# Optimization experiments

Measured on AMD Instinct MI355X. Metric: run time of the kernel, lower is better.

The kernel has to match this reference:

```python
import jax, jax.numpy as jnp
import numpy as np

EPS = 1e-5
PROJ_EPS = 1e-5
MAX_TANH_ARG = 15.0
NUM_LAYERS = 2

def _norm(x):
    return jnp.sqrt(jnp.sum(x * x, axis=-1, keepdims=True))

def log_map_zero(y):
    # Poincare ball log map at the origin: arctanh(||y||) * y / ||y||
    n = _norm(y)
    n_c = jnp.clip(n, EPS, 1.0 - PROJ_EPS)
    return jnp.arctanh(n_c) * y / jnp.maximum(n, EPS)

def exp_map_zero(v):
    # Poincare ball exp map at the origin: tanh(||v||) * v / ||v||
    n = _norm(v)
    n_c = jnp.clip(n, EPS, MAX_TANH_ARG)
    return jnp.tanh(n_c) * v / jnp.maximum(n, EPS)

def setup_inputs() -> dict:
    key = jax.random.key(0)
    k1, k2, k3, k4 = jax.random.split(key, 4)
    N, K, D = 50000, 32, 128
    # scale initial features so they lie inside the unit ball
    node_repr = jax.random.normal(k1, (N, D), dtype=jnp.float32) * 0.01
    adj_mat = jax.random.randint(k2, (N, K), 0, N, dtype=jnp.int32)
    weight = jax.random.uniform(k3, (N, K), dtype=jnp.float32)
    mask = jnp.ones((N, 1), dtype=jnp.float32)
    # learned params: one [D, D] matrix per layer (tie_weight=False, poincare)
    msg_weights = jax.random.normal(k4, (NUM_LAYERS, D, D), dtype=jnp.float32) * (1.0 / np.sqrt(D))
    return {"node_repr": node_repr, "adj_mat": adj_mat, "weight": weight,
            "mask": mask, "msg_weights": msg_weights}

def reference(node_repr, adj_mat, weight, mask, msg_weights):
    x = node_repr
    for step in range(NUM_LAYERS):
        # log map back to tangent space at origin (identity on first layer)
        x = (log_map_zero(x) if step > 0 else x) * mask
        msg = (x @ msg_weights[step]) * mask            # [N, D] dense projection
        nbr = msg[adj_mat]                              # [N, K, D] gather by adjacency
        combined = jnp.einsum('nk,nkd->nd', weight, nbr) * mask  # weighted neighbor sum (dropout p=0)
        x = exp_map_zero(combined) * mask               # back to the manifold
        x = jax.nn.relu(x) * mask                       # poincare activation
    return x
```

## Files before the change

kernel.cpp:

```cpp
#include <hip/hip_runtime.h>

#define EPS 1e-5f
#define PROJ_EPS 1e-5f
#define MAX_TANH_ARG 15.0f

typedef __bf16 bf16x8 __attribute__((ext_vector_type(8)));
typedef float f32x4 __attribute__((ext_vector_type(4)));
typedef float f32x2 __attribute__((ext_vector_type(2)));

__device__ __forceinline__ unsigned short f2bf(float f) {
  unsigned u = __builtin_bit_cast(unsigned, f);
  u += 0x7fffu + ((u >> 16) & 1u);
  return (unsigned short)(u >> 16);
}
__device__ __forceinline__ float bf2f(unsigned short h) {
  return __builtin_bit_cast(float, ((unsigned)h) << 16);
}

union BF8 {
  unsigned short u[8];
  bf16x8 v;
  uint4 q;
};

__global__ void pack_w_kernel(const float* __restrict__ W,
                              unsigned short* __restrict__ wpack) {
  int tid = blockIdx.x * blockDim.x + threadIdx.x;
  if (tid >= 2 * 8 * 4 * 64) return;
  int lane = tid & 63;
  int s = (tid >> 6) & 3;
  int t = (tid >> 8) & 7;
  int layer = tid >> 11;
  int quad = lane >> 4;
  int n = t * 16 + (lane & 15);
  unsigned short* dst = wpack + ((size_t)((layer * 32 + t * 4 + s) * 64 + lane)) * 8;
  const float* src = W + (size_t)layer * 16384;
#pragma unroll
  for (int j = 0; j < 8; ++j) {
    int k = s * 32 + quad * 8 + j;
    dst[j] = f2bf(src[(size_t)k * 128 + n]);
  }
}

template <int MODE>
__global__ __launch_bounds__(256) void gemm_kernel(
    const float* __restrict__ xf, const unsigned short* __restrict__ xb,
    const float* __restrict__ rowscale, const unsigned short* __restrict__ wpack,
    unsigned short* __restrict__ msg, int N) {
  __shared__ unsigned short tile[64][136];
  const int lane = threadIdx.x & 63;
  const int wv = threadIdx.x >> 6;
  const int m = lane & 15;
  const int quad = lane >> 4;
  const int base = blockIdx.x * 64;
  const int wbase = base + wv * 16;
  const int row = wbase + m;
  const int rowc = row < N ? row : N - 1;

  f32x4 acc[8];
#pragma unroll
  for (int t = 0; t < 8; ++t) acc[t] = (f32x4){0.f, 0.f, 0.f, 0.f};

#pragma unroll
  for (int sk = 0; sk < 4; ++sk) {
    const int k0 = sk * 32 + quad * 8;
    BF8 a;
    if (MODE == 0) {
      const float4* xp = (const float4*)(xf + (size_t)rowc * 128 + k0);
      float4 p0 = xp[0], p1 = xp[1];
      a.u[0] = f2bf(p0.x); a.u[1] = f2bf(p0.y);
      a.u[2] = f2bf(p0.z); a.u[3] = f2bf(p0.w);
      a.u[4] = f2bf(p1.x); a.u[5] = f2bf(p1.y);
      a.u[6] = f2bf(p1.z); a.u[7] = f2bf(p1.w);
    } else {
      a.q = *(const uint4*)(xb + (size_t)rowc * 128 + k0);
    }
#pragma unroll
    for (int t = 0; t < 8; ++t) {
      BF8 b;
      b.q = *(const uint4*)(wpack + (size_t)((t * 4 + sk) * 64 + lane) * 8);
      acc[t] = __builtin_amdgcn_mfma_f32_16x16x32_bf16(a.v, b.v, acc[t], 0, 0, 0);
    }
  }

  float sc[4];
#pragma unroll
  for (int r = 0; r < 4; ++r) {
    int rr = wbase + quad * 4 + r;
    rr = rr < N ? rr : N - 1;
    float s = rowscale[rr];
    sc[r] = (MODE == 0) ? s * s : s;
  }
#pragma unroll
  for (int t = 0; t < 8; ++t) {
    const int c = t * 16 + m;
#pragma unroll
    for (int r = 0; r < 4; ++r) {
      tile[wv * 16 + quad * 4 + r][c] = f2bf(acc[t][r] * sc[r]);
    }
  }
  __syncthreads();

#pragma unroll
  for (int i = 0; i < 4; ++i) {
    const int flat = i * 4096 + (int)threadIdx.x * 16;
    const int r64 = flat >> 8;
    const int colb = flat & 255;
    const int grow = base + r64;
    if (grow < N) {
      *(uint4*)((char*)msg + (size_t)grow * 256 + colb) =
          *(const uint4*)&tile[r64][colb >> 1];
    }
  }
}

template <int MODE>
__global__ __launch_bounds__(256) void gather_kernel(
    const unsigned short* __restrict__ msg, const int* __restrict__ adj,
    const float* __restrict__ wgt, const float* __restrict__ mask,
    unsigned short* __restrict__ x1out, float* __restrict__ lsout,
    float* __restrict__ out, int N) {
  const int lane = threadIdx.x & 63;
  const int half = lane >> 5;
  const int j = lane & 31;
  const int gw = (int)((blockIdx.x * blockDim.x + threadIdx.x) >> 6);
  const int nw = (int)((gridDim.x * blockDim.x) >> 6);
  const int npairs = (N + 1) >> 1;

  for (int p = gw; p < npairs; p += nw) {
    const int nA = p * 2;
    const int nB = nA + 1;
    const int myn = nA + half;
    int idxv = 0;
    float wv = 0.f;
    if (myn < N) {
      idxv = adj[(size_t)myn * 32 + j];
      wv = wgt[(size_t)myn * 32 + j];
    }
    f32x2 aA = {0.f, 0.f}, aB = {0.f, 0.f};
#pragma unroll
    for (int k = 0; k < 32; ++k) {
      const int idA = __builtin_amdgcn_readlane(idxv, k);
      const float wA = __builtin_bit_cast(
          float, __builtin_amdgcn_readlane(__builtin_bit_cast(int, wv), k));
      const int idB = __builtin_amdgcn_readlane(idxv, 32 + k);
      const float wB = __builtin_bit_cast(
          float, __builtin_amdgcn_readlane(__builtin_bit_cast(int, wv), 32 + k));
      const unsigned prA = *(const unsigned*)(msg + (size_t)idA * 128 + 2 * lane);
      const unsigned prB = *(const unsigned*)(msg + (size_t)idB * 128 + 2 * lane);
      f32x2 mA, mB;
      mA.x = __builtin_bit_cast(float, prA << 16);
      mA.y = __builtin_bit_cast(float, prA & 0xffff0000u);
      mB.x = __builtin_bit_cast(float, prB << 16);
      mB.y = __builtin_bit_cast(float, prB & 0xffff0000u);
      aA = __builtin_elementwise_fma(mA, (f32x2){wA, wA}, aA);
      aB = __builtin_elementwise_fma(mB, (f32x2){wB, wB}, aB);
    }

#pragma unroll
    for (int which = 0; which < 2; ++which) {
      const int n = which ? nB : nA;
      if (n >= N) continue;
      const f32x2 a = which ? aB : aA;
      const float mm = mask[n];
      const float c0 = a.x * mm, c1 = a.y * mm;
      float s2 = c0 * c0 + c1 * c1;
#pragma unroll
      for (int o = 32; o > 0; o >>= 1) s2 += __shfl_xor(s2, o);
      const float nrm = sqrtf(s2);
      const float ncl = fminf(fmaxf(nrm, EPS), MAX_TANH_ARG);
      const float esc = tanhf(ncl) / fmaxf(nrm, EPS) * mm;
      const float v0 = fmaxf(esc * c0, 0.f) * mm;
      const float v1 = fmaxf(esc * c1, 0.f) * mm;
      if (MODE == 0) {
        const unsigned pk = (unsigned)f2bf(v0) | ((unsigned)f2bf(v1) << 16);
        *(unsigned*)(x1out + (size_t)n * 128 + 2 * lane) = pk;
        float r2 = v0 * v0 + v1 * v1;
#pragma unroll
        for (int o = 32; o > 0; o >>= 1) r2 += __shfl_xor(r2, o);
        const float nr = sqrtf(r2);
        const float nc2 = fminf(fmaxf(nr, EPS), 1.0f - PROJ_EPS);
        const float ls = 0.5f * logf((1.0f + nc2) / (1.0f - nc2)) / fmaxf(nr, EPS);
        if (lane == 0) lsout[n] = ls * mm * mm;
      } else {
        *(float2*)(out + (size_t)n * 128 + 2 * lane) = make_float2(v0, v1);
      }
    }
  }
}

extern "C" void kernel_launch(void* const* d_in, const int* in_sizes, int n_in,
                              void* d_out, int out_size, void* d_ws, size_t ws_size,
                              hipStream_t stream) {
  const float* node = (const float*)d_in[0];
  const int* adj = (const int*)d_in[1];
  const float* wgt = (const float*)d_in[2];
  const float* mask = (const float*)d_in[3];
  const float* mw = (const float*)d_in[4];
  float* out = (float*)d_out;
  const int N = in_sizes[0] / 128;

  char* ws = (char*)d_ws;
  unsigned short* wpack = (unsigned short*)ws;
  float* lsp = (float*)(ws + 65536);
  size_t ls_bytes = ((size_t)N * 4 + 255) & ~(size_t)255;
  unsigned short* msg = (unsigned short*)(ws + 65536 + ls_bytes);
  unsigned short* x1 = (unsigned short*)d_out;

  hipLaunchKernelGGL(pack_w_kernel, dim3(16), dim3(256), 0, stream, mw, wpack);
  const int gb = (N + 63) / 64;
  hipLaunchKernelGGL((gemm_kernel<0>), dim3(gb), dim3(256), 0, stream,
                     node, (const unsigned short*)nullptr, mask, wpack, msg, N);
  hipLaunchKernelGGL((gather_kernel<0>), dim3(2048), dim3(256), 0, stream,
                     msg, adj, wgt, mask, x1, lsp, (float*)nullptr, N);
  hipLaunchKernelGGL((gemm_kernel<1>), dim3(gb), dim3(256), 0, stream,
                     (const float*)nullptr, x1, lsp, wpack + 16384, msg, N);
  hipLaunchKernelGGL((gather_kernel<1>), dim3(2048), dim3(256), 0, stream,
                     msg, adj, wgt, mask, (unsigned short*)nullptr, (float*)nullptr, out, N);
}
```

Measured before the change: 216.8 us.

## Split message matrix into column planes and gather with 16-byte loads per lane

The GEMM now writes messages into four column planes of 64 bytes per row. The gather kernel stages adjacency indices and weights in shared memory, then gives each node 4 lanes that issue 16-byte loads from one plane at a time. This replaces the old scheme of one wave per node pair doing 4-byte loads per lane. The goal is fewer, wider memory requests and better L2 locality, since each plane is a quarter the size of the full matrix. The cost is more registers per thread (32 accumulators) and shorter norm reductions that now rely on shuffles across 4 lanes.

```diff
diff --git a/kernel.cpp b/kernel.cpp
--- a/kernel.cpp
+++ b/kernel.cpp
@@ -12,9 +12,6 @@
   unsigned u = __builtin_bit_cast(unsigned, f);
   u += 0x7fffu + ((u >> 16) & 1u);
   return (unsigned short)(u >> 16);
-}
-__device__ __forceinline__ float bf2f(unsigned short h) {
-  return __builtin_bit_cast(float, ((unsigned)h) << 16);
 }
 
 union BF8 {
@@ -46,7 +43,7 @@
 __global__ __launch_bounds__(256) void gemm_kernel(
     const float* __restrict__ xf, const unsigned short* __restrict__ xb,
     const float* __restrict__ rowscale, const unsigned short* __restrict__ wpack,
-    unsigned short* __restrict__ msg, int N) {
+    unsigned short* __restrict__ msg4, int N, int planeBytes) {
   __shared__ unsigned short tile[64][136];
   const int lane = threadIdx.x & 63;
   const int wv = threadIdx.x >> 6;
@@ -108,7 +105,9 @@
     const int colb = flat & 255;
     const int grow = base + r64;
     if (grow < N) {
-      *(uint4*)((char*)msg + (size_t)grow * 256 + colb) =
+      const int plane = colb >> 6;
+      const int within = colb & 63;
+      *(uint4*)((char*)msg4 + (size_t)plane * planeBytes + (size_t)grow * 64 + within) =
           *(const uint4*)&tile[r64][colb >> 1];
     }
   }
@@ -116,74 +115,117 @@
 
 template <int MODE>
 __global__ __launch_bounds__(256) void gather_kernel(
-    const unsigned short* __restrict__ msg, const int* __restrict__ adj,
+    const unsigned short* __restrict__ msg4, const int* __restrict__ adj,
     const float* __restrict__ wgt, const float* __restrict__ mask,
     unsigned short* __restrict__ x1out, float* __restrict__ lsout,
-    float* __restrict__ out, int N) {
-  const int lane = threadIdx.x & 63;
-  const int half = lane >> 5;
-  const int j = lane & 31;
-  const int gw = (int)((blockIdx.x * blockDim.x + threadIdx.x) >> 6);
-  const int nw = (int)((gridDim.x * blockDim.x) >> 6);
-  const int npairs = (N + 1) >> 1;
-
-  for (int p = gw; p < npairs; p += nw) {
-    const int nA = p * 2;
-    const int nB = nA + 1;
-    const int myn = nA + half;
-    int idxv = 0;
-    float wv = 0.f;
-    if (myn < N) {
-      idxv = adj[(size_t)myn * 32 + j];
-      wv = wgt[(size_t)myn * 32 + j];
-    }
-    f32x2 aA = {0.f, 0.f}, aB = {0.f, 0.f};
-#pragma unroll
+    float* __restrict__ out, int N, int planeHW) {
+  __shared__ unsigned long long pairs[64 * 33];
+  const int t = threadIdx.x;
+  const int lane = t & 63;
+  const int wv = t >> 6;
+  const int g = lane >> 2;
+  const int sub = lane & 3;
+  const int nbase = blockIdx.x * 64;
+
+  for (int e = t; e < 64 * 32; e += 256) {
+    const int node = e >> 5, k = e & 31;
+    const int gn = nbase + node;
+    int id = 0;
+    float w = 0.f;
+    if (gn < N) {
+      id = adj[(size_t)gn * 32 + k];
+      w = wgt[(size_t)gn * 32 + k];
+    }
+    pairs[node * 33 + k] = (unsigned long long)(unsigned)id |
+        ((unsigned long long)__builtin_bit_cast(unsigned, w) << 32);
+  }
+  __syncthreads();
+
+  const int mynode = wv * 16 + g;
+  const int gnode = nbase + mynode;
+  const unsigned long long* mp = pairs + mynode * 33;
+  const int suboff = sub * 16;
+
+  f32x2 acc[16];
+#pragma unroll
+  for (int i = 0; i < 16; ++i) acc[i] = (f32x2){0.f, 0.f};
+
+#pragma unroll
+  for (int p = 0; p < 4; ++p) {
+    const char* plane = (const char*)(msg4 + (size_t)p * planeHW);
+#pragma unroll 8
     for (int k = 0; k < 32; ++k) {
-      const int idA = __builtin_amdgcn_readlane(idxv, k);
-      const float wA = __builtin_bit_cast(
-          float, __builtin_amdgcn_readlane(__builtin_bit_cast(int, wv), k));
-      const int idB = __builtin_amdgcn_readlane(idxv, 32 + k);
-      const float wB = __builtin_bit_cast(
-          float, __builtin_amdgcn_readlane(__builtin_bit_cast(int, wv), 32 + k));
-      const unsigned prA = *(const unsigned*)(msg + (size_t)idA * 128 + 2 * lane);
-      const unsigned prB = *(const unsigned*)(msg + (size_t)idB * 128 + 2 * lane);
-      f32x2 mA, mB;
-      mA.x = __builtin_bit_cast(float, prA << 16);
-      mA.y = __builtin_bit_cast(float, prA & 0xffff0000u);
-      mB.x = __builtin_bit_cast(float, prB << 16);
-      mB.y = __builtin_bit_cast(float, prB & 0xffff0000u);
-      aA = __builtin_elementwise_fma(mA, (f32x2){wA, wA}, aA);
-      aB = __builtin_elementwise_fma(mB, (f32x2){wB, wB}, aB);
-    }
-
-#pragma unroll
-    for (int which = 0; which < 2; ++which) {
-      const int n = which ? nB : nA;
-      if (n >= N) continue;
-      const f32x2 a = which ? aB : aA;
-      const float mm = mask[n];
-      const float c0 = a.x * mm, c1 = a.y * mm;
-      float s2 = c0 * c0 + c1 * c1;
-#pragma unroll
-      for (int o = 32; o > 0; o >>= 1) s2 += __shfl_xor(s2, o);
-      const float nrm = sqrtf(s2);
-      const float ncl = fminf(fmaxf(nrm, EPS), MAX_TANH_ARG);
-      const float esc = tanhf(ncl) / fmaxf(nrm, EPS) * mm;
-      const float v0 = fmaxf(esc * c0, 0.f) * mm;
-      const float v1 = fmaxf(esc * c1, 0.f) * mm;
-      if (MODE == 0) {
-        const unsigned pk = (unsigned)f2bf(v0) | ((unsigned)f2bf(v1) << 16);
-        *(unsigned*)(x1out + (size_t)n * 128 + 2 * lane) = pk;
-        float r2 = v0 * v0 + v1 * v1;
-#pragma unroll
-        for (int o = 32; o > 0; o >>= 1) r2 += __shfl_xor(r2, o);
+      const unsigned long long pk = mp[k];
+      const unsigned id = (unsigned)pk;
+      const float w = __builtin_bit_cast(float, (unsigned)(pk >> 32));
+      const uint4 q = *(const uint4*)(plane + ((size_t)id * 64 + suboff));
+      const f32x2 w2 = {w, w};
+#pragma unroll
+      for (int d = 0; d < 4; ++d) {
+        const unsigned qd = (&q.x)[d];
+        f32x2 v2;
+        v2.x = __builtin_bit_cast(float, qd << 16);
+        v2.y = __builtin_bit_cast(float, qd & 0xffff0000u);
+        acc[p * 4 + d] = __builtin_elementwise_fma(v2, w2, acc[p * 4 + d]);
+      }
+    }
+  }
+
+  const int gcl = gnode < N ? gnode : N - 1;
+  const float mm = mask[gcl];
+  float s2 = 0.f;
+#pragma unroll
+  for (int i = 0; i < 16; ++i) {
+    acc[i].x *= mm;
+    acc[i].y *= mm;
+    s2 = fmaf(acc[i].x, acc[i].x, s2);
+    s2 = fmaf(acc[i].y, acc[i].y, s2);
+  }
+  s2 += __shfl_xor(s2, 1);
+  s2 += __shfl_xor(s2, 2);
+  const float nrm = sqrtf(s2);
+  const float ncl = fminf(fmaxf(nrm, EPS), MAX_TANH_ARG);
+  const float esc = tanhf(ncl) / fmaxf(nrm, EPS) * mm;
+  float v[32];
+#pragma unroll
+  for (int i = 0; i < 16; ++i) {
+    v[2 * i] = fmaxf(esc * acc[i].x, 0.f) * mm;
+    v[2 * i + 1] = fmaxf(esc * acc[i].y, 0.f) * mm;
+  }
+
+  if (MODE == 0) {
+    float r2 = 0.f;
+#pragma unroll
+    for (int i = 0; i < 32; ++i) r2 = fmaf(v[i], v[i], r2);
+    r2 += __shfl_xor(r2, 1);
+    r2 += __shfl_xor(r2, 2);
+    if (gnode < N) {
+#pragma unroll
+      for (int p = 0; p < 4; ++p) {
+        uint4 pk4;
+        unsigned* pw = &pk4.x;
+#pragma unroll
+        for (int d = 0; d < 4; ++d)
+          pw[d] = (unsigned)f2bf(v[p * 8 + d * 2]) |
+                  ((unsigned)f2bf(v[p * 8 + d * 2 + 1]) << 16);
+        *(uint4*)((char*)x1out + (size_t)gnode * 256 + p * 64 + suboff) = pk4;
+      }
+      if (sub == 0) {
         const float nr = sqrtf(r2);
         const float nc2 = fminf(fmaxf(nr, EPS), 1.0f - PROJ_EPS);
-        const float ls = 0.5f * logf((1.0f + nc2) / (1.0f - nc2)) / fmaxf(nr, EPS);
-        if (lane == 0) lsout[n] = ls * mm * mm;
-      } else {
-        *(float2*)(out + (size_t)n * 128 + 2 * lane) = make_float2(v0, v1);
+        const float ls = 0.5f * logf((1.f + nc2) / (1.f - nc2)) / fmaxf(nr, EPS);
+        lsout[gnode] = ls * mm * mm;
+      }
+    }
+  } else {
+    if (gnode < N) {
+#pragma unroll
+      for (int p = 0; p < 4; ++p) {
+        const int cb = p * 32 + sub * 8;
+        *(float4*)(out + (size_t)gnode * 128 + cb) =
+            make_float4(v[p * 8 + 0], v[p * 8 + 1], v[p * 8 + 2], v[p * 8 + 3]);
+        *(float4*)(out + (size_t)gnode * 128 + cb + 4) =
+            make_float4(v[p * 8 + 4], v[p * 8 + 5], v[p * 8 + 6], v[p * 8 + 7]);
       }
     }
   }
@@ -200,21 +242,24 @@
   float* out = (float*)d_out;
   const int N = in_sizes[0] / 128;
 
+  const int gb = (N + 63) / 64;
+  const int planeBytes = gb * 64 * 64;
+  const int planeHW = planeBytes / 2;
+
   char* ws = (char*)d_ws;
   unsigned short* wpack = (unsigned short*)ws;
   float* lsp = (float*)(ws + 65536);
   size_t ls_bytes = ((size_t)N * 4 + 255) & ~(size_t)255;
-  unsigned short* msg = (unsigned short*)(ws + 65536 + ls_bytes);
+  unsigned short* msg4 = (unsigned short*)(ws + 65536 + ls_bytes);
   unsigned short* x1 = (unsigned short*)d_out;
 
   hipLaunchKernelGGL(pack_w_kernel, dim3(16), dim3(256), 0, stream, mw, wpack);
-  const int gb = (N + 63) / 64;
   hipLaunchKernelGGL((gemm_kernel<0>), dim3(gb), dim3(256), 0, stream,
-                     node, (const unsigned short*)nullptr, mask, wpack, msg, N);
-  hipLaunchKernelGGL((gather_kernel<0>), dim3(2048), dim3(256), 0, stream,
-                     msg, adj, wgt, mask, x1, lsp, (float*)nullptr, N);
+                     node, (const unsigned short*)nullptr, mask, wpack, msg4, N, planeBytes);
+  hipLaunchKernelGGL((gather_kernel<0>), dim3(gb), dim3(256), 0, stream,
+                     msg4, adj, wgt, mask, x1, lsp, (float*)nullptr, N, planeHW);
   hipLaunchKernelGGL((gemm_kernel<1>), dim3(gb), dim3(256), 0, stream,
-                     (const float*)nullptr, x1, lsp, wpack + 16384, msg, N);
-  hipLaunchKernelGGL((gather_kernel<1>), dim3(2048), dim3(256), 0, stream,
-                     msg, adj, wgt, mask, (unsigned short*)nullptr, (float*)nullptr, out, N);
-}
+                     (const float*)nullptr, x1, lsp, wpack + 16384, msg4, N, planeBytes);
+  hipLaunchKernelGGL((gather_kernel<1>), dim3(gb), dim3(256), 0, stream,
+                     msg4, adj, wgt, mask, (unsigned short*)nullptr, (float*)nullptr, out, N, planeHW);
+}
```

Result: no change. 213.4 us (-1.5%).
